# Kernel tuning notes

Measured on AMD Instinct MI355X. Metric: run time of the kernel, lower is better.

Reference implementation:

```python
import jax, jax.numpy as jnp
import numpy as np
import math

B, SQ, SKV = 8, 1024, 1024
D, H, DQ, DV = 1024, 16, 64, 64
EPS = 1e-3  # Keras LayerNormalization default epsilon
IN_DECODER = True


def _layer_norm(x, gamma, beta):
    m = jnp.mean(x, axis=-1, keepdims=True)
    v = jnp.mean((x - m) ** 2, axis=-1, keepdims=True)
    return gamma * (x - m) / jnp.sqrt(v + EPS) + beta


def setup_inputs() -> dict:
    key = jax.random.key(0)
    ks = jax.random.split(key, 6)
    x = jax.random.normal(ks[0], (B, SQ, D), dtype=jnp.float32)
    # self-attention: query and key/value sequences are the same tensor
    lengths = jax.random.randint(ks[1], (B,), SKV // 2, SKV + 1, dtype=jnp.int32)
    init = 0.02
    Wq = jax.random.normal(ks[2], (D, H * DQ), dtype=jnp.float32) * init
    Wkv = jax.random.normal(ks[3], (D, H * (DQ + DV)), dtype=jnp.float32) * init
    Wo = jax.random.normal(ks[4], (H * DV, D), dtype=jnp.float32) * init
    return {
        "query_sequences": x,
        "key_value_sequences": x,
        "key_value_sequence_lengths": lengths,
        "Wq": Wq, "bq": jnp.zeros((H * DQ,), jnp.float32),
        "Wkv": Wkv, "bkv": jnp.zeros((H * (DQ + DV),), jnp.float32),
        "Wo": Wo, "bo": jnp.zeros((D,), jnp.float32),
        "ln_gamma": jnp.ones((D,), jnp.float32),
        "ln_beta": jnp.zeros((D,), jnp.float32),
    }


def reference(query_sequences, key_value_sequences, key_value_sequence_lengths,
              Wq, bq, Wkv, bkv, Wo, bo, ln_gamma, ln_beta):
    # detect self-attention exactly as the original (elementwise equality)
    self_attn = jnp.all(query_sequences == key_value_sequences)
    q_seq = _layer_norm(query_sequences, ln_gamma, ln_beta)
    kv_ln = _layer_norm(key_value_sequences, ln_gamma, ln_beta)
    kv_seq = jnp.where(self_attn, kv_ln, key_value_sequences)
    residual = q_seq  # pre-norm residual (original adds post-LN queries)

    q = (q_seq @ Wq + bq).reshape(B, SQ, H, DQ).transpose(0, 2, 1, 3)   # b h q d
    kvp = kv_seq @ Wkv + bkv
    k = kvp[..., : H * DQ].reshape(B, SKV, H, DQ).transpose(0, 2, 1, 3)  # b h k d
    v = kvp[..., H * DQ:].reshape(B, SKV, H, DV).transpose(0, 2, 1, 3)   # b h k d

    scores = jnp.einsum("bhqd,bhkd->bhqk", q, k) / math.sqrt(DQ)
    # padding mask on keys
    not_pad = (jnp.arange(SKV)[None, None, None, :]
               < key_value_sequence_lengths[:, None, None, None])
    scores = jnp.where(not_pad, scores, -jnp.inf)
    if IN_DECODER:
        causal = jnp.tril(jnp.ones((SQ, SKV), dtype=bool))[None, None]
        scores = jnp.where(jnp.logical_or(~self_attn, causal), scores, -jnp.inf)

    attn = jax.nn.softmax(scores, axis=-1)  # dropout is identity in eval mode
    out = jnp.einsum("bhqk,bhkd->bhqd", attn, v)
    out = out.transpose(0, 2, 1, 3).reshape(B, SQ, H * DV)
    out = out @ Wo + bo
    return out + residual
```

## Files before the change

kernel.cpp:

```cpp
#include <hip/hip_runtime.h>

typedef unsigned short u16;
typedef unsigned int u32;
typedef __attribute__((ext_vector_type(8))) short short8;
typedef __attribute__((ext_vector_type(4))) float fx4;

#define LOG2E 1.44269504088896340736f

__device__ __forceinline__ u16 f2bf(float f) {
    unsigned int u = __float_as_uint(f);
    u += 0x7fffu + ((u >> 16) & 1u);
    return (u16)(u >> 16);
}

__device__ __forceinline__ float bf2f(u16 v) {
    u32 u = ((u32)v) << 16;
    return __uint_as_float(u);
}

__device__ __forceinline__ u32 pack_bf2(float lo, float hi) {
    return __builtin_amdgcn_perm(__float_as_uint(hi), __float_as_uint(lo), 0x07060302u);
}

__device__ __forceinline__ float fast_exp2(float x) {
#if __has_builtin(__builtin_amdgcn_exp2f)
    return __builtin_amdgcn_exp2f(x);
#else
    return exp2f(x);
#endif
}

__device__ __forceinline__ fx4 mfma16(short8 a, short8 b, fx4 c) {
    return __builtin_amdgcn_mfma_f32_16x16x32_bf16(a, b, c, 0, 0, 0);
}

__device__ __forceinline__ void gload_lds16(const u16* g, u16* l) {
    __builtin_amdgcn_global_load_lds(
        (const __attribute__((address_space(1))) void*)g,
        (__attribute__((address_space(3))) void*)l, 16, 0, 0);
}

__global__ __launch_bounds__(256) void ln_wt_kernel(
    const float* __restrict__ x, const float* __restrict__ gamma,
    const float* __restrict__ beta, u16* __restrict__ yb,
    const float* __restrict__ Wq, const float* __restrict__ Wkv,
    const float* __restrict__ Wo, u16* __restrict__ Wt) {
    int blk = blockIdx.x;
    if (blk < 2048) {
        int wave = threadIdx.x >> 6, lane = threadIdx.x & 63;
        int row = (blk << 2) + wave;
        const float* xr = x + ((size_t)row << 10);
        float4 v[4];
        float s = 0.0f, sq = 0.0f;
#pragma unroll
        for (int i = 0; i < 4; ++i) {
            v[i] = *(const float4*)(xr + (i << 8) + (lane << 2));
            s  += v[i].x + v[i].y + v[i].z + v[i].w;
            sq += v[i].x * v[i].x + v[i].y * v[i].y + v[i].z * v[i].z + v[i].w * v[i].w;
        }
#pragma unroll
        for (int o = 32; o > 0; o >>= 1) {
            s  += __shfl_xor(s, o, 64);
            sq += __shfl_xor(sq, o, 64);
        }
        float mean = s * (1.0f / 1024.0f);
        float var  = sq * (1.0f / 1024.0f) - mean * mean;
        float rstd = rsqrtf(var + 1e-3f);
#pragma unroll
        for (int i = 0; i < 4; ++i) {
            int off = (i << 8) + (lane << 2);
            float4 g  = *(const float4*)(gamma + off);
            float4 bb = *(const float4*)(beta + off);
            float4 y;
            y.x = (v[i].x - mean) * rstd * g.x + bb.x;
            y.y = (v[i].y - mean) * rstd * g.y + bb.y;
            y.z = (v[i].z - mean) * rstd * g.z + bb.z;
            y.w = (v[i].w - mean) * rstd * g.w + bb.w;
            unsigned long long p = (unsigned long long)f2bf(y.x)
                | ((unsigned long long)f2bf(y.y) << 16)
                | ((unsigned long long)f2bf(y.z) << 32)
                | ((unsigned long long)f2bf(y.w) << 48);
            *(unsigned long long*)(yb + ((size_t)row << 10) + off) = p;
        }
    } else {
        int wtb = blk - 2048;
        int n0 = (wtb & 127) << 5;
        int k0 = (wtb >> 7) << 5;
        const float* W; int sn0, SN;
        if (n0 < 1024)      { W = Wq;  sn0 = n0;        SN = 1024; }
        else if (n0 < 3072) { W = Wkv; sn0 = n0 - 1024; SN = 2048; }
        else                { W = Wo;  sn0 = n0 - 3072; SN = 1024; }
        __shared__ float tile[32][33];
        int tx = threadIdx.x & 31, ty = threadIdx.x >> 5;
#pragma unroll
        for (int r = 0; r < 4; ++r)
            tile[ty + r * 8][tx] = W[(size_t)(k0 + ty + r * 8) * SN + sn0 + tx];
        __syncthreads();
#pragma unroll
        for (int r = 0; r < 4; ++r)
            Wt[(size_t)(n0 + ty + r * 8) * 1024 + k0 + tx] = f2bf(tile[tx][ty + r * 8]);
    }
}

template <int MODE, int WMT>
__global__ __launch_bounds__(256) void gemm_bt(
    const u16* __restrict__ A, const u16* __restrict__ Bt,
    const float* __restrict__ bq, const float* __restrict__ bkv,
    const u16* __restrict__ resb, float* __restrict__ Cf, u16* __restrict__ Cb,
    u16* __restrict__ Vt, int M, int N, int K, float qscale) {
    __shared__ __align__(16) u16 sA[WMT * 32 * 64];
    __shared__ __align__(16) u16 sB[128 * 64];

    int nx = gridDim.x;
    int total = nx * gridDim.y;
    int id0 = blockIdx.x + blockIdx.y * nx;
    int nid = (id0 & 7) * (total >> 3) + (id0 >> 3);
    int bx = nid % nx, by = nid / nx;
    int m0 = by * (WMT * 32), n0 = bx << 7;

    int tid = threadIdx.x, lane = tid & 63, wave = tid >> 6;
    int quad = lane >> 4, l15 = lane & 15, swr = lane & 7;
    int wm = (wave >> 1) * (WMT * 16), wn = (wave & 1) << 6;
    int srow = lane >> 3;
    int gseg = (lane & 7) ^ srow;

    fx4 acc[WMT][4];
    fx4 zero = {0.0f, 0.0f, 0.0f, 0.0f};
#pragma unroll
    for (int i = 0; i < WMT; ++i)
#pragma unroll
        for (int j = 0; j < 4; ++j) acc[i][j] = zero;

    const u16* aSrc[WMT];
    const u16* bSrc[4];
    u16* aDst[WMT];
    u16* bDst[4];
#pragma unroll
    for (int t = 0; t < WMT; ++t) {
        int cA = wave * WMT + t;
        int rowA = (cA << 3) + srow;
        aSrc[t] = A + (size_t)(m0 + rowA) * K + (gseg << 3);
        aDst[t] = &sA[cA << 9];
    }
#pragma unroll
    for (int t = 0; t < 4; ++t) {
        int cB = (wave << 2) + t;
        int rowB = (cB << 3) + srow;
        bSrc[t] = Bt + (size_t)(n0 + rowB) * K + (gseg << 3);
        bDst[t] = &sB[cB << 9];
    }

    for (int k0 = 0; k0 < K; k0 += 64) {
#pragma unroll
        for (int t = 0; t < WMT; ++t) {
            gload_lds16(aSrc[t], aDst[t]);
            aSrc[t] += 64;
            if (t < 4) {
                gload_lds16(bSrc[t], bDst[t]);
                bSrc[t] += 64;
            }
        }
        __syncthreads();
#pragma unroll
        for (int kk = 0; kk < 64; kk += 32) {
            int ks = (kk >> 3) + quad;
            short8 af[WMT], bf[4];
#pragma unroll
            for (int mt = 0; mt < WMT; ++mt) {
                int r = wm + (mt << 4) + l15;
                af[mt] = *(const short8*)&sA[(r << 6) + (((ks ^ swr) & 7) << 3)];
            }
#pragma unroll
            for (int nt = 0; nt < 4; ++nt) {
                int r = wn + (nt << 4) + l15;
                bf[nt] = *(const short8*)&sB[(r << 6) + (((ks ^ swr) & 7) << 3)];
            }
#pragma unroll
            for (int mt = 0; mt < WMT; ++mt)
#pragma unroll
                for (int nt = 0; nt < 4; ++nt)
                    acc[mt][nt] = mfma16(af[mt], bf[nt], acc[mt][nt]);
        }
        __syncthreads();
    }

    if (MODE == 0 && n0 >= 2048) {
#pragma unroll
        for (int mt = 0; mt < WMT; ++mt)
#pragma unroll
            for (int nt = 0; nt < 4; ++nt)
#pragma unroll
                for (int r = 0; r < 4; ++r) {
                    int row = m0 + wm + (mt << 4) + (quad << 2) + r;
                    int col = n0 + wn + (nt << 4) + l15;
                    float v = acc[mt][nt][r] + bkv[col - 1024];
                    int bb = row >> 10, k = row & 1023;
                    int h = (col - 2048) >> 6, d = col & 63;
                    int kt = k >> 6, kin = k & 63;
                    int kp = ((kin & 15) << 2) | (kin >> 4);
                    Vt[(size_t)((((bb << 4) + h) << 6) + d) * 1024
                       + (kt << 6) + kp] = f2bf(v);
                }
        return;
    }

#pragma unroll
    for (int mt = 0; mt < WMT; ++mt)
#pragma unroll
        for (int nt = 0; nt < 4; ++nt)
#pragma unroll
            for (int r = 0; r < 4; ++r) {
                int row = m0 + wm + (mt << 4) + (quad << 2) + r;
                int col = n0 + wn + (nt << 4) + l15;
                if (MODE == 1) {
                    float v = acc[mt][nt][r] + bq[col];
                    size_t idx = (size_t)row * N + col;
                    Cf[idx] = v + bf2f(resb[idx]);
                } else {
                    float bias = (col < 1024) ? bq[col] : bkv[col - 1024];
                    float v = acc[mt][nt][r] + bias;
                    if (col < 1024) v *= qscale;
                    Cb[(size_t)row * N + col] = f2bf(v);
                }
            }
}

__global__ __launch_bounds__(256) void attn_kernel(
    const u16* __restrict__ QKVp, const u16* __restrict__ Vt,
    const int* __restrict__ lens, u16* __restrict__ O) {
    int id0 = blockIdx.x + (blockIdx.y << 7);
    int nid = ((id0 & 7) << 6) + (id0 >> 3);
    int bh = nid >> 2;
    int j = nid & 3;
    int b = bh >> 4, h = bh & 15;
    int len = lens[b];
    int cap = (len - 1) >> 6;
    int tid = threadIdx.x, lane = tid & 63, w = tid >> 6;
    int quad = lane >> 4, l15 = lane & 15;

    __shared__ __align__(16) u16 sK[2][64 * 64];
    __shared__ __align__(16) u16 sV[2][64 * 64];
    __shared__ __align__(16) u16 sP[4 * 2048];
    u16* sPw = &sP[w << 11];

    int lrow = lane >> 3;
    int lseg = lane & 7;

    auto stage = [&](int kt, int buf) {
        int k0g = kt << 6;
#pragma unroll
        for (int i = 0; i < 2; ++i) {
            int row = (w << 4) + (i << 3) + lrow;
            int gs = lseg ^ (row & 7);
            gload_lds16(QKVp + (size_t)((b << 10) + k0g + row) * 3072
                           + 1024 + (h << 6) + (gs << 3),
                        &sK[buf][((w << 1) + i) << 9]);
            gload_lds16(Vt + (size_t)((bh << 6) + row) * 1024
                           + k0g + (gs << 3),
                        &sV[buf][((w << 1) + i) << 9]);
        }
    };

    fx4 zero = {0.0f, 0.0f, 0.0f, 0.0f};

#pragma unroll
    for (int phase = 0; phase < 2; ++phase) {
        int s = phase ? (7 - j) : j;
        int q0 = s << 7;
        int wq0 = q0 + (w << 5);
        int ktend_blk = min((q0 + 127) >> 6, cap);
        int ktend_w   = min((wq0 + 31) >> 6, cap);

        short8 qf[2][2];
#pragma unroll
        for (int mt = 0; mt < 2; ++mt)
#pragma unroll
            for (int kk = 0; kk < 2; ++kk) {
                int qrow = (b << 10) + wq0 + (mt << 4) + l15;
                qf[mt][kk] = *(const short8*)(QKVp + (size_t)qrow * 3072
                              + (h << 6) + (kk << 5) + (quad << 3));
            }

        fx4 oacc[2][4];
        float lsum[2][4];
#pragma unroll
        for (int mt = 0; mt < 2; ++mt)
#pragma unroll
            for (int nt = 0; nt < 4; ++nt) oacc[mt][nt] = zero;
#pragma unroll
        for (int mt = 0; mt < 2; ++mt)
#pragma unroll
            for (int r = 0; r < 4; ++r) lsum[mt][r] = 0.0f;

        stage(0, 0);
        __syncthreads();

        for (int kt = 0; kt <= ktend_blk; ++kt) {
            int cb = kt & 1;
            if (kt < ktend_blk) stage(kt + 1, cb ^ 1);

            if (kt <= ktend_w) {
                int k0g = kt << 6;
                fx4 sacc[2][4];
#pragma unroll
                for (int mt = 0; mt < 2; ++mt)
#pragma unroll
                    for (int nt = 0; nt < 4; ++nt) sacc[mt][nt] = zero;
#pragma unroll
                for (int kk = 0; kk < 2; ++kk) {
                    int seg = (kk << 2) + quad;
                    short8 kf[4];
#pragma unroll
                    for (int nt = 0; nt < 4; ++nt) {
                        int row = (nt << 4) + l15;
                        kf[nt] = *(const short8*)&sK[cb][(row << 6)
                                   + (((seg ^ (row & 7)) & 7) << 3)];
                    }
#pragma unroll
                    for (int mt = 0; mt < 2; ++mt)
#pragma unroll
                        for (int nt = 0; nt < 4; ++nt)
                            sacc[mt][nt] = mfma16(qf[mt][kk], kf[nt], sacc[mt][nt]);
                }

                bool needm = ((k0g + 63) > wq0) || ((k0g + 64) > len);
                if (needm) {
#pragma unroll
                    for (int mt = 0; mt < 2; ++mt)
#pragma unroll
                        for (int nt = 0; nt < 4; ++nt) {
                            int kg = k0g + (nt << 4) + l15;
#pragma unroll
                            for (int r = 0; r < 4; ++r) {
                                int qr = wq0 + (mt << 4) + (quad << 2) + r;
                                if (kg > qr || kg >= len)
                                    sacc[mt][nt][r] = -30000.0f;
                            }
                        }
                }

#pragma unroll
                for (int mt = 0; mt < 2; ++mt) {
#pragma unroll
                    for (int nt = 0; nt < 4; ++nt)
#pragma unroll
                        for (int r = 0; r < 4; ++r)
                            sacc[mt][nt][r] = fast_exp2(sacc[mt][nt][r]);
#pragma unroll
                    for (int r = 0; r < 4; ++r) {
                        lsum[mt][r] += (sacc[mt][0][r] + sacc[mt][1][r])
                                     + (sacc[mt][2][r] + sacc[mt][3][r]);
                        int row = (mt << 4) + (quad << 2) + r;
                        u32 lo = pack_bf2(sacc[mt][0][r], sacc[mt][1][r]);
                        u32 hi = pack_bf2(sacc[mt][2][r], sacc[mt][3][r]);
                        uint2 pv; pv.x = lo; pv.y = hi;
                        int addr = (row << 6)
                                 + (((((l15 >> 1)) ^ (row & 7)) & 7) << 3)
                                 + ((l15 & 1) << 2);
                        *(uint2*)&sPw[addr] = pv;
                    }
                }
                __builtin_amdgcn_s_waitcnt(0xC07F);

#pragma unroll
                for (int kk = 0; kk < 2; ++kk) {
                    int seg = (kk << 2) + quad;
                    short8 vf[4], pf[2];
#pragma unroll
                    for (int nt = 0; nt < 4; ++nt) {
                        int row = (nt << 4) + l15;
                        vf[nt] = *(const short8*)&sV[cb][(row << 6)
                                   + (((seg ^ (row & 7)) & 7) << 3)];
                    }
#pragma unroll
                    for (int mt = 0; mt < 2; ++mt) {
                        int row = (mt << 4) + l15;
                        pf[mt] = *(const short8*)&sPw[(row << 6)
                                   + (((seg ^ (row & 7)) & 7) << 3)];
                    }
#pragma unroll
                    for (int mt = 0; mt < 2; ++mt)
#pragma unroll
                        for (int nt = 0; nt < 4; ++nt)
                            oacc[mt][nt] = mfma16(pf[mt], vf[nt], oacc[mt][nt]);
                }
            }
            __syncthreads();
        }

#pragma unroll
        for (int mt = 0; mt < 2; ++mt)
#pragma unroll
            for (int r = 0; r < 4; ++r) {
                float v = lsum[mt][r];
                v += __shfl_xor(v, 1, 64);
                v += __shfl_xor(v, 2, 64);
                v += __shfl_xor(v, 4, 64);
                v += __shfl_xor(v, 8, 64);
                lsum[mt][r] = __builtin_amdgcn_rcpf(v);
            }
#pragma unroll
        for (int mt = 0; mt < 2; ++mt)
#pragma unroll
            for (int nt = 0; nt < 4; ++nt)
#pragma unroll
                for (int r = 0; r < 4; ++r) {
                    int row = (b << 10) + wq0 + (mt << 4) + (quad << 2) + r;
                    int col = (h << 6) + (nt << 4) + l15;
                    O[((size_t)row << 10) + col] =
                        f2bf(oacc[mt][nt][r] * lsum[mt][r]);
                }
    }
}

extern "C" void kernel_launch(void* const* d_in, const int* in_sizes, int n_in,
                              void* d_out, int out_size, void* d_ws, size_t ws_size,
                              hipStream_t stream) {
    (void)in_sizes; (void)n_in; (void)out_size; (void)ws_size;
    const float* x    = (const float*)d_in[0];
    const int*   lens = (const int*)d_in[2];
    const float* Wq   = (const float*)d_in[3];
    const float* bq   = (const float*)d_in[4];
    const float* Wkv  = (const float*)d_in[5];
    const float* bkv  = (const float*)d_in[6];
    const float* Wo   = (const float*)d_in[7];
    const float* bo   = (const float*)d_in[8];
    const float* gam  = (const float*)d_in[9];
    const float* bet  = (const float*)d_in[10];
    float* out = (float*)d_out;

    char* w = (char*)d_ws;
    u16* xln_b  = (u16*)w;  w += (size_t)8192 * 1024 * 2;
    u16* Wall_t = (u16*)w;  w += (size_t)4096 * 1024 * 2;
    u16* QKVp   = (u16*)w;  w += (size_t)8192 * 3072 * 2;
    u16* Vt     = (u16*)w;  w += (size_t)8192 * 1024 * 2;
    u16* AO     = (u16*)w;  w += (size_t)8192 * 1024 * 2;

    ln_wt_kernel<<<6144, 256, 0, stream>>>(x, gam, bet, xln_b, Wq, Wkv, Wo, Wall_t);
    gemm_bt<0, 4><<<dim3(24, 64), 256, 0, stream>>>(xln_b, Wall_t, bq, bkv,
        nullptr, nullptr, QKVp, Vt, 8192, 3072, 1024, 0.125f * LOG2E);
    attn_kernel<<<dim3(128, 4), 256, 0, stream>>>(QKVp, Vt, lens, AO);
    gemm_bt<1, 4><<<dim3(8, 64), 256, 0, stream>>>(AO, Wall_t + (size_t)3072 * 1024,
        bo, nullptr, xln_b, out, nullptr, nullptr, 8192, 1024, 1024, 1.0f);
}
```

Before: 260.3 us.

## Load K/V fragments directly from global memory and drop GEMM block swizzle

The attention kernel no longer stages K and V tiles into double-buffered shared memory with block-wide barriers. Each wave instead reads its MFMA K and V fragments straight from global memory (relying on cache) and iterates only up to its own causal limit, with no __syncthreads. Separately, the GEMM drops its blockIdx remapping in favour of plain grid indexing. The aim is to remove barrier stalls and LDS traffic, at the cost of redundant global/L2 reads across the four waves, less latency hiding, and worse cache locality for the GEMM.

```diff
diff --git a/kernel.cpp b/kernel.cpp
--- a/kernel.cpp
+++ b/kernel.cpp
@@ -110,14 +110,7 @@
     u16* __restrict__ Vt, int M, int N, int K, float qscale) {
     __shared__ __align__(16) u16 sA[WMT * 32 * 64];
     __shared__ __align__(16) u16 sB[128 * 64];
-
-    int nx = gridDim.x;
-    int total = nx * gridDim.y;
-    int id0 = blockIdx.x + blockIdx.y * nx;
-    int nid = (id0 & 7) * (total >> 3) + (id0 >> 3);
-    int bx = nid % nx, by = nid / nx;
-    int m0 = by * (WMT * 32), n0 = bx << 7;
-
+    int m0 = blockIdx.y * (WMT * 32), n0 = blockIdx.x << 7;
     int tid = threadIdx.x, lane = tid & 63, wave = tid >> 6;
     int quad = lane >> 4, l15 = lane & 15, swr = lane & 7;
     int wm = (wave >> 1) * (WMT * 16), wn = (wave & 1) << 6;
@@ -238,38 +231,20 @@
     int tid = threadIdx.x, lane = tid & 63, w = tid >> 6;
     int quad = lane >> 4, l15 = lane & 15;
 
-    __shared__ __align__(16) u16 sK[2][64 * 64];
-    __shared__ __align__(16) u16 sV[2][64 * 64];
     __shared__ __align__(16) u16 sP[4 * 2048];
     u16* sPw = &sP[w << 11];
 
-    int lrow = lane >> 3;
-    int lseg = lane & 7;
-
-    auto stage = [&](int kt, int buf) {
-        int k0g = kt << 6;
-#pragma unroll
-        for (int i = 0; i < 2; ++i) {
-            int row = (w << 4) + (i << 3) + lrow;
-            int gs = lseg ^ (row & 7);
-            gload_lds16(QKVp + (size_t)((b << 10) + k0g + row) * 3072
-                           + 1024 + (h << 6) + (gs << 3),
-                        &sK[buf][((w << 1) + i) << 9]);
-            gload_lds16(Vt + (size_t)((bh << 6) + row) * 1024
-                           + k0g + (gs << 3),
-                        &sV[buf][((w << 1) + i) << 9]);
-        }
-    };
-
     fx4 zero = {0.0f, 0.0f, 0.0f, 0.0f};
+
+    const u16* Kbase = QKVp + (size_t)(b << 10) * 3072 + 1024 + (h << 6);
+    const u16* Vbase = Vt + (size_t)(bh << 6) * 1024;
 
 #pragma unroll
     for (int phase = 0; phase < 2; ++phase) {
         int s = phase ? (7 - j) : j;
         int q0 = s << 7;
         int wq0 = q0 + (w << 5);
-        int ktend_blk = min((q0 + 127) >> 6, cap);
-        int ktend_w   = min((wq0 + 31) >> 6, cap);
+        int ktend_w = min((wq0 + 31) >> 6, cap);
 
         short8 qf[2][2];
 #pragma unroll
@@ -292,100 +267,91 @@
 #pragma unroll
             for (int r = 0; r < 4; ++r) lsum[mt][r] = 0.0f;
 
-        stage(0, 0);
-        __syncthreads();
-
-        for (int kt = 0; kt <= ktend_blk; ++kt) {
-            int cb = kt & 1;
-            if (kt < ktend_blk) stage(kt + 1, cb ^ 1);
-
-            if (kt <= ktend_w) {
-                int k0g = kt << 6;
-                fx4 sacc[2][4];
+        for (int kt = 0; kt <= ktend_w; ++kt) {
+            int k0g = kt << 6;
+            fx4 sacc[2][4];
+#pragma unroll
+            for (int mt = 0; mt < 2; ++mt)
+#pragma unroll
+                for (int nt = 0; nt < 4; ++nt) sacc[mt][nt] = zero;
+#pragma unroll
+            for (int kk = 0; kk < 2; ++kk) {
+                int seg = (kk << 2) + quad;
+                short8 kf[4];
+#pragma unroll
+                for (int nt = 0; nt < 4; ++nt) {
+                    int krow = k0g + (nt << 4) + l15;
+                    kf[nt] = *(const short8*)(Kbase + (size_t)krow * 3072
+                               + (seg << 3));
+                }
 #pragma unroll
                 for (int mt = 0; mt < 2; ++mt)
 #pragma unroll
-                    for (int nt = 0; nt < 4; ++nt) sacc[mt][nt] = zero;
-#pragma unroll
-                for (int kk = 0; kk < 2; ++kk) {
-                    int seg = (kk << 2) + quad;
-                    short8 kf[4];
+                    for (int nt = 0; nt < 4; ++nt)
+                        sacc[mt][nt] = mfma16(qf[mt][kk], kf[nt], sacc[mt][nt]);
+            }
+
+            bool needm = ((k0g + 63) > wq0) || ((k0g + 64) > len);
+            if (needm) {
+#pragma unroll
+                for (int mt = 0; mt < 2; ++mt)
 #pragma unroll
                     for (int nt = 0; nt < 4; ++nt) {
-                        int row = (nt << 4) + l15;
-                        kf[nt] = *(const short8*)&sK[cb][(row << 6)
-                                   + (((seg ^ (row & 7)) & 7) << 3)];
+                        int kg = k0g + (nt << 4) + l15;
+#pragma unroll
+                        for (int r = 0; r < 4; ++r) {
+                            int qr = wq0 + (mt << 4) + (quad << 2) + r;
+                            if (kg > qr || kg >= len)
+                                sacc[mt][nt][r] = -30000.0f;
+                        }
                     }
-#pragma unroll
-                    for (int mt = 0; mt < 2; ++mt)
-#pragma unroll
-                        for (int nt = 0; nt < 4; ++nt)
-                            sacc[mt][nt] = mfma16(qf[mt][kk], kf[nt], sacc[mt][nt]);
-                }
-
-                bool needm = ((k0g + 63) > wq0) || ((k0g + 64) > len);
-                if (needm) {
-#pragma unroll
-                    for (int mt = 0; mt < 2; ++mt)
-#pragma unroll
-                        for (int nt = 0; nt < 4; ++nt) {
-                            int kg = k0g + (nt << 4) + l15;
-#pragma unroll
-                            for (int r = 0; r < 4; ++r) {
-                                int qr = wq0 + (mt << 4) + (quad << 2) + r;
-                                if (kg > qr || kg >= len)
-                                    sacc[mt][nt][r] = -30000.0f;
-                            }
-                        }
-                }
-
+            }
+
+#pragma unroll
+            for (int mt = 0; mt < 2; ++mt) {
+#pragma unroll
+                for (int nt = 0; nt < 4; ++nt)
+#pragma unroll
+                    for (int r = 0; r < 4; ++r)
+                        sacc[mt][nt][r] = fast_exp2(sacc[mt][nt][r]);
+#pragma unroll
+                for (int r = 0; r < 4; ++r) {
+                    lsum[mt][r] += (sacc[mt][0][r] + sacc[mt][1][r])
+                                 + (sacc[mt][2][r] + sacc[mt][3][r]);
+                    int row = (mt << 4) + (quad << 2) + r;
+                    u32 lo = pack_bf2(sacc[mt][0][r], sacc[mt][1][r]);
+                    u32 hi = pack_bf2(sacc[mt][2][r], sacc[mt][3][r]);
+                    uint2 pv; pv.x = lo; pv.y = hi;
+                    int addr = (row << 6)
+                             + (((((l15 >> 1)) ^ (row & 7)) & 7) << 3)
+                             + ((l15 & 1) << 2);
+                    *(uint2*)&sPw[addr] = pv;
+                }
+            }
+            __builtin_amdgcn_s_waitcnt(0xC07F);
+
+#pragma unroll
+            for (int kk = 0; kk < 2; ++kk) {
+                int seg = (kk << 2) + quad;
+                short8 vf[4], pf[2];
+#pragma unroll
+                for (int nt = 0; nt < 4; ++nt) {
+                    int drow = (nt << 4) + l15;
+                    vf[nt] = *(const short8*)(Vbase + (size_t)drow * 1024
+                               + k0g + (seg << 3));
+                }
 #pragma unroll
                 for (int mt = 0; mt < 2; ++mt) {
+                    int row = (mt << 4) + l15;
+                    pf[mt] = *(const short8*)&sPw[(row << 6)
+                               + (((seg ^ (row & 7)) & 7) << 3)];
+                }
+#pragma unroll
+                for (int mt = 0; mt < 2; ++mt)
 #pragma unroll
                     for (int nt = 0; nt < 4; ++nt)
-#pragma unroll
-                        for (int r = 0; r < 4; ++r)
-                            sacc[mt][nt][r] = fast_exp2(sacc[mt][nt][r]);
-#pragma unroll
-                    for (int r = 0; r < 4; ++r) {
-                        lsum[mt][r] += (sacc[mt][0][r] + sacc[mt][1][r])
-                                     + (sacc[mt][2][r] + sacc[mt][3][r]);
-                        int row = (mt << 4) + (quad << 2) + r;
-                        u32 lo = pack_bf2(sacc[mt][0][r], sacc[mt][1][r]);
-                        u32 hi = pack_bf2(sacc[mt][2][r], sacc[mt][3][r]);
-                        uint2 pv; pv.x = lo; pv.y = hi;
-                        int addr = (row << 6)
-                                 + (((((l15 >> 1)) ^ (row & 7)) & 7) << 3)
-                                 + ((l15 & 1) << 2);
-                        *(uint2*)&sPw[addr] = pv;
-                    }
-                }
-                __builtin_amdgcn_s_waitcnt(0xC07F);
-
-#pragma unroll
-                for (int kk = 0; kk < 2; ++kk) {
-                    int seg = (kk << 2) + quad;
-                    short8 vf[4], pf[2];
-#pragma unroll
-                    for (int nt = 0; nt < 4; ++nt) {
-                        int row = (nt << 4) + l15;
-                        vf[nt] = *(const short8*)&sV[cb][(row << 6)
-                                   + (((seg ^ (row & 7)) & 7) << 3)];
-                    }
-#pragma unroll
-                    for (int mt = 0; mt < 2; ++mt) {
-                        int row = (mt << 4) + l15;
-                        pf[mt] = *(const short8*)&sPw[(row << 6)
-                                   + (((seg ^ (row & 7)) & 7) << 3)];
-                    }
-#pragma unroll
-                    for (int mt = 0; mt < 2; ++mt)
-#pragma unroll
-                        for (int nt = 0; nt < 4; ++nt)
-                            oacc[mt][nt] = mfma16(pf[mt], vf[nt], oacc[mt][nt]);
-                }
-            }
-            __syncthreads();
+                        oacc[mt][nt] = mfma16(pf[mt], vf[nt], oacc[mt][nt]);
+            }
         }
 
 #pragma unroll
```

Result: slower. 290.5 us (+11.6%).
